# Performance work log

Hardware: AMD Instinct MI355X
Metric: run time of the kernel (lower is better)

## Reference

```python
import jax, jax.numpy as jnp
import numpy as np

B, N, L, E, U, G, R, D, C = 64, 50000, 8, 100000, 20000, 20000, 64, 16, 2


def setup_inputs() -> dict:
    rng = np.random.default_rng(0)
    key = jax.random.key(0)
    ks = jax.random.split(key, 10)
    # index structures (duplicate-free where the torch code assumes uniqueness)
    gene_map = jnp.asarray(rng.choice(N, G, replace=False).astype(np.int32))
    dst_unique = jnp.stack([jnp.asarray(rng.choice(N, U, replace=False).astype(np.int32)) for _ in range(L)])
    root_ids = jnp.asarray(rng.choice(N, R, replace=False).astype(np.int32))
    src = jax.random.randint(ks[0], (L, E), 0, N, dtype=jnp.int32)
    dst_pos = jax.random.randint(ks[1], (L, E), 0, U, dtype=jnp.int32)
    # data and parameters
    X_gene_batch = jax.random.normal(ks[2], (B, G), jnp.float32)
    w_in = jax.random.normal(ks[3], (D,), jnp.float32) * 0.5   # Linear(1, d) weight
    b_in = jax.random.normal(ks[4], (D,), jnp.float32) * 0.1
    W = jax.random.normal(ks[5], (L, D, D), jnp.float32) * (1.0 / np.sqrt(D))  # xavier-ish
    bias = jnp.zeros((N, D), jnp.float32)
    W_head = jax.random.normal(ks[6], (C, R * D), jnp.float32) * (1.0 / np.sqrt(R * D))
    b_head = jnp.zeros((C,), jnp.float32)
    return {
        "X_gene_batch": X_gene_batch, "w_in": w_in, "b_in": b_in, "W": W,
        "bias": bias, "W_head": W_head, "b_head": b_head,
        "gene_map": gene_map, "src": src, "dst_pos": dst_pos,
        "dst_unique": dst_unique, "root_ids": root_ids,
    }


def reference(X_gene_batch, w_in, b_in, W, bias, W_head, b_head,
              gene_map, src, dst_pos, dst_unique, root_ids):
    Bn = X_gene_batch.shape[0]
    n_nodes, d = bias.shape
    n_layers = W.shape[0]
    u = dst_unique.shape[1]
    # _init_state_vector: h=0, scatter in_proj(X[...,None]) at gene_map
    gene_emb = X_gene_batch[..., None] * w_in + b_in          # [B, G, d]
    h = jnp.zeros((Bn, n_nodes, d), X_gene_batch.dtype)
    h = h.at[:, gene_map].set(gene_emb)
    for li in range(n_layers):
        h_src = h[:, src[li]]                                  # gather [B, E, d]
        msg = jnp.einsum('bed,df->bef', h_src, W[li])          # small dxd matmul
        agg = jnp.zeros((Bn, u, d), h.dtype).at[:, dst_pos[li]].add(msg)  # scatter-add
        h_dst = jnp.tanh(agg + bias[dst_unique[li]][None])     # bias lookup + tanh (dropout=0)
        h = h.at[:, dst_unique[li]].set(h_dst)                 # write back
    feat = h[:, root_ids].reshape(Bn, -1)                      # roots_concat readout
    return feat @ W_head.T + b_head                            # [B, C]
```

## Files before the change

kernel.cpp:

```cpp
#include <hip/hip_runtime.h>
#include <hip/hip_fp16.h>
#include <cmath>

constexpr int B_ = 64, N_ = 50000, L_ = 8, E_ = 100000, U_ = 20000, G_ = 20000, R_ = 64, D_ = 16, C_ = 2;
constexpr int EPL_ = E_ + 3 * U_ + 4096;
constexpr int EPLG_ = EPL_ / 4 + 64;
constexpr int GPW = 8;
constexpr int GCAP = EPL_ / 4;
constexpr int SW = (GCAP + GPW - 1) / GPW;
constexpr int HISTB = (E_ + 255) / 256;

constexpr int BC = 64;
constexpr int F = BC * 2;

constexpr int HBC = 32;
constexpr int FH = HBC * 2;
constexpr int DST0 = 1 + G_;
constexpr int AROWS = DST0 + L_ * U_;

__device__ __forceinline__ float tanh_fast(float x) {
  float e = __expf(2.0f * x);
  return 1.0f - 2.0f * __builtin_amdgcn_rcpf(e + 1.0f);
}


__global__ __launch_bounds__(256) void hist_mark_k(
    const int* __restrict__ dst_pos, int* __restrict__ cnt,
    const int* __restrict__ dst_unique, const int* __restrict__ gene_map,
    int* __restrict__ wmask, int* __restrict__ posarr, int* __restrict__ lw0) {
  int li = blockIdx.y;
  int bx = blockIdx.x;
  if (bx < HISTB) {
    int e = bx * 256 + threadIdx.x;
    if (e < E_) atomicAdd(&cnt[li * U_ + dst_pos[li * E_ + e]], 1);
  } else if (li == 0) {
    int t = (bx - HISTB) * 256 + threadIdx.x;
    if (t < L_ * U_) {
      int lj = t / U_, u = t % U_;
      int n = dst_unique[t];
      posarr[lj * N_ + n] = u;
      atomicOr(&wmask[n], 1 << lj);
    } else {
      int g = t - L_ * U_;
      if (g < G_) lw0[gene_map[g]] = 1 + g;
    }
  }
}

__global__ __launch_bounds__(1024) void scan_kernel(
    const int* __restrict__ cnt, int* __restrict__ offs,
    int* __restrict__ woffs) {
  __shared__ int sums[1024];
  int li = blockIdx.x, t = threadIdx.x;
  int base = t * 20;
  int v[20];
  int s = 0;
#pragma unroll
  for (int i = 0; i < 20; ++i) {
    int idx = base + i;
    int c = (idx < U_) ? cnt[li * U_ + idx] : -1;
    int pc = (c < 0) ? 0 : ((c == 0) ? 4 : ((c + 3) & ~3));
    v[i] = s;
    s += pc;
  }
  sums[t] = s;
  __syncthreads();
  for (int off = 1; off < 1024; off <<= 1) {
    int o = (t >= off) ? sums[t - off] : 0;
    __syncthreads();
    sums[t] += o;
    __syncthreads();
  }
  int excl = sums[t] - s;
#pragma unroll
  for (int i = 0; i < 20; ++i) {
    int idx = base + i;
    if (idx < U_) {
      int sv = excl + v[i];
      offs[li * (U_ + 1) + idx] = sv;
      woffs[li * (U_ + 1) + idx] = sv;
    }
  }
  if (t == 1023) offs[li * (U_ + 1) + U_] = sums[1023];
}

__global__ __launch_bounds__(256) void scatter_arena_k(
    const int* __restrict__ dst_pos, const int* __restrict__ src,
    int* __restrict__ woffs, const int* __restrict__ wmask,
    const int* __restrict__ posarr, const int* __restrict__ lw0,
    int* __restrict__ ssrc) {
  int e = blockIdx.x * 256 + threadIdx.x;
  int li = blockIdx.y;
  if (e >= E_) return;
  int u = dst_pos[li * E_ + e];
  int p = atomicAdd(&woffs[li * (U_ + 1) + u], 1);
  int s = src[li * E_ + e];
  int m = wmask[s] & ((1 << li) - 1);
  int phys;
  if (m) {
    int lj = 31 - __clz(m);
    phys = DST0 + lj * U_ + posarr[lj * N_ + s];
  } else {
    phys = lw0[s];
  }
  ssrc[(size_t)li * EPL_ + p] = phys;
}

__global__ __launch_bounds__(256) void scatter_classic_k(
    const int* __restrict__ dst_pos, const int* __restrict__ src,
    int* __restrict__ woffs, int* __restrict__ ssrc) {
  int e = blockIdx.x * 256 + threadIdx.x;
  int li = blockIdx.y;
  if (e >= E_) return;
  int u = dst_pos[li * E_ + e];
  int p = atomicAdd(&woffs[li * (U_ + 1) + u], 1);
  ssrc[(size_t)li * EPL_ + p] = src[li * E_ + e];
}

__global__ __launch_bounds__(256) void pad_fill_ug_k(
    const int* __restrict__ woffs, const int* __restrict__ offs,
    int* __restrict__ ssrc, int* __restrict__ ug, int sentinel,
    float4* __restrict__ zrow) {
  int t = blockIdx.x * 256 + threadIdx.x;
  if (t < L_ * U_) {
    int li = t / U_, u = t % U_;
    int start = offs[li * (U_ + 1) + u];
    int end = woffs[li * (U_ + 1) + u];
    int pend = offs[li * (U_ + 1) + u + 1];
    int* sp = ssrc + (size_t)li * EPL_;
    for (int p = end; p < pend; ++p) sp[p] = sentinel;
    int* ugp = ug + (size_t)li * EPLG_;
    for (int g = start >> 2; g < (pend >> 2); ++g) ugp[g] = u;
  } else {
    int t2 = t - L_ * U_;
    int li = t2 >> 10, j = t2 & 1023;
    if (li < L_) {
      int* sp = ssrc + (size_t)li * EPL_;
      int ptot = offs[li * (U_ + 1) + U_];
      if (j < 256) {
        int pos = ptot + j;
        if (pos < EPL_) sp[pos] = sentinel;
        sp[EPL_ - 256 + j] = sentinel;
      }
      int* ugp = ug + (size_t)li * EPLG_;
      for (int gq = (ptot >> 2) + j; gq < EPLG_; gq += 1024) ugp[gq] = -1;
      if (li == 0 && j < FH && zrow) zrow[j] = make_float4(0.f, 0.f, 0.f, 0.f);
    }
  }
}

#define PHASE(VACC, VLD, IDLD, IDPF, NUCUR)          \
  {                                                  \
    loadRows(VLD, IDLD);                             \
    IDPF = *(const int4*)(sp + 4 * CLG(g + 4));      \
    int nuCur = NUCUR;                               \
    NUCUR = ugp[CLG(g + 3) + 1];                     \
    accum(VACC);                                     \
    if (nuCur != curU) {                             \
      flushu(curU);                                  \
      if (g + 1 >= gstop) return;                    \
      curU = nuCur;                                  \
    }                                                \
    ++g;                                             \
  }


__global__ __launch_bounds__(256) void gene_a(
    const float* __restrict__ X, const float* __restrict__ w_in,
    const float* __restrict__ b_in, float4* __restrict__ h4, int half) {
  __shared__ float xs[8][33];
  int tid = threadIdx.x;
  int g0 = blockIdx.x * 8;
  {
    int b = tid >> 3, gi = tid & 7;
    xs[gi][b] = X[(size_t)(half * HBC + b) * G_ + g0 + gi];
  }
  __syncthreads();
  int b = tid & 31;
  int gi = tid >> 5;
  float x = xs[gi][b];
  int g = g0 + gi;
  float4 out[2];
  __half2* oh = reinterpret_cast<__half2*>(out);
#pragma unroll
  for (int k = 0; k < 8; ++k) {
    float r0 = fmaf(x, w_in[2 * k], b_in[2 * k]);
    float r1 = fmaf(x, w_in[2 * k + 1], b_in[2 * k + 1]);
    oh[k] = __float22half2_rn(make_float2(r0, r1));
  }
  h4[(size_t)(1 + g) * FH + b * 2] = out[0];
  h4[(size_t)(1 + g) * FH + b * 2 + 1] = out[1];
}

__global__ __launch_bounds__(256, 2) void gfused_a(
    const float4* __restrict__ h4, const int* __restrict__ ug,
    const int* __restrict__ ssrc, const float* __restrict__ W,
    const float* __restrict__ bias, const int* __restrict__ dst_unique,
    float4* __restrict__ o4, int li) {
  __shared__ float Wlds[256];
  int tid = threadIdx.x;
  Wlds[tid] = W[li * 256 + tid];
  __syncthreads();
  int lane = tid & 63;
  int dh = lane & 1;
  int wv = __builtin_amdgcn_readfirstlane(blockIdx.x * 4 + (tid >> 6));
  const int* ugp = ug + (size_t)li * EPLG_;
  const int* sp = ssrc + (size_t)li * EPL_;
  const int* du = dst_unique + (size_t)li * U_;

  int g0 = wv * GPW, gend = g0 + GPW;
  int prevU = (g0 == 0) ? -2 : ugp[g0 - 1];
  int g = g0;
  while (g < gend && ugp[g] == prevU) ++g;
  if (g >= gend) return;
  int curU = ugp[g];
  if (curU < 0) return;
  int uend = ugp[gend - 1];
  int gstop;
  if (uend < 0) {
    gstop = g;
    while (ugp[gstop] >= 0) ++gstop;
  } else {
    gstop = gend;
    while (ugp[gstop] == uend) ++gstop;
  }

  __half2 acc[2][4];
  const __half2 z = __half2half2(__float2half(0.f));
#pragma unroll
  for (int j = 0; j < 2; ++j)
#pragma unroll
    for (int k = 0; k < 4; ++k) acc[j][k] = z;

  auto flushu = [&](int u) {
    int node = du[u];
    float biasv[8];
    {
      const float4* bp = (const float4*)(bias + (size_t)node * 16 + dh * 8);
      float4 q0 = bp[0], q1 = bp[1];
      biasv[0] = q0.x; biasv[1] = q0.y; biasv[2] = q0.z; biasv[3] = q0.w;
      biasv[4] = q1.x; biasv[5] = q1.y; biasv[6] = q1.z; biasv[7] = q1.w;
    }
    float a8[8];
#pragma unroll
    for (int k = 0; k < 4; ++k) {
      float2 f0 = __half22float2(acc[0][k]);
      float2 f1 = __half22float2(acc[1][k]);
      __half2 hv = __float22half2_rn(make_float2(f0.x + f1.x, f0.y + f1.y));
      float2 fa = __half22float2(hv);
      a8[2 * k] = fa.x; a8[2 * k + 1] = fa.y;
    }
    float pm[16];
#pragma unroll
    for (int j = 0; j < 16; ++j) pm[j] = 0.f;
#pragma unroll
    for (int dd = 0; dd < 8; ++dd) {
      float s = a8[dd];
      const float4* wr = (const float4*)&Wlds[(dh * 8 + dd) * 16];
      float4 w0 = wr[0], w1 = wr[1], w2 = wr[2], w3 = wr[3];
      pm[0] = fmaf(s, w0.x, pm[0]);  pm[1] = fmaf(s, w0.y, pm[1]);
      pm[2] = fmaf(s, w0.z, pm[2]);  pm[3] = fmaf(s, w0.w, pm[3]);
      pm[4] = fmaf(s, w1.x, pm[4]);  pm[5] = fmaf(s, w1.y, pm[5]);
      pm[6] = fmaf(s, w1.z, pm[6]);  pm[7] = fmaf(s, w1.w, pm[7]);
      pm[8] = fmaf(s, w2.x, pm[8]);  pm[9] = fmaf(s, w2.y, pm[9]);
      pm[10] = fmaf(s, w2.z, pm[10]); pm[11] = fmaf(s, w2.w, pm[11]);
      pm[12] = fmaf(s, w3.x, pm[12]); pm[13] = fmaf(s, w3.y, pm[13]);
      pm[14] = fmaf(s, w3.z, pm[14]); pm[15] = fmaf(s, w3.w, pm[15]);
    }
    float m8[8];
#pragma unroll
    for (int jj = 0; jj < 8; ++jj) {
      float s0 = pm[jj] + __shfl_xor(pm[jj], 1, 64);
      float s1 = pm[8 + jj] + __shfl_xor(pm[8 + jj], 1, 64);
      m8[jj] = dh ? s1 : s0;
    }
    float4 outv;
    __half2* ov = reinterpret_cast<__half2*>(&outv);
#pragma unroll
    for (int k = 0; k < 4; ++k) {
      ov[k] = __float22half2_rn(
          make_float2(tanh_fast(m8[2 * k] + biasv[2 * k]),
                      tanh_fast(m8[2 * k + 1] + biasv[2 * k + 1])));
    }
    o4[(size_t)(DST0 + li * U_ + u) * FH + lane] = outv;
#pragma unroll
    for (int j = 0; j < 2; ++j)
#pragma unroll
      for (int k = 0; k < 4; ++k) acc[j][k] = z;
  };

  auto loadRows = [&](float4 (&v)[4], int4 id) {
    v[0] = h4[(size_t)id.x * FH + lane];
    v[1] = h4[(size_t)id.y * FH + lane];
    v[2] = h4[(size_t)id.z * FH + lane];
    v[3] = h4[(size_t)id.w * FH + lane];
  };
  auto accum = [&](const float4 (&v)[4]) {
#pragma unroll
    for (int j = 0; j < 4; ++j) {
      const __half2* p = reinterpret_cast<const __half2*>(&v[j]);
#pragma unroll
      for (int k = 0; k < 4; ++k)
        acc[j & 1][k] = __hadd2(acc[j & 1][k], p[k]);
    }
  };
  auto CLG = [&](int q) { return (q < GCAP) ? q : GCAP - 1; };

  int4 id0 = *(const int4*)(sp + 4 * g);
  int4 id1 = *(const int4*)(sp + 4 * CLG(g + 1));
  int4 idP = *(const int4*)(sp + 4 * CLG(g + 2));
  int4 idQ = *(const int4*)(sp + 4 * CLG(g + 3));
  int4 idR;
  int nuA = ugp[g + 1];
  int nuB = ugp[CLG(g + 1) + 1];
  int nuC = ugp[CLG(g + 2) + 1];

  float4 va[4], vb[4], vc[4];
  loadRows(va, id0);
  loadRows(vb, id1);

  for (;;) {
    PHASE(va, vc, idP, idR, nuA)
    PHASE(vb, va, idQ, idP, nuB)
    PHASE(vc, vb, idR, idQ, nuC)
  }
}

__global__ __launch_bounds__(64) void head_a(
    const float4* __restrict__ h4, const float* __restrict__ W_head,
    const float* __restrict__ b_head, const int* __restrict__ root_ids,
    const int* __restrict__ wmask, const int* __restrict__ posarr,
    const int* __restrict__ lw0, int half, float* __restrict__ out) {
  int bl = blockIdx.x;
  int r = threadIdx.x;
  int node = root_ids[r];
  int m = wmask[node];
  int phys;
  if (m) {
    int lj = 31 - __clz(m);
    phys = DST0 + lj * U_ + posarr[lj * N_ + node];
  } else {
    phys = lw0[node];
  }
  float4 p0 = h4[(size_t)phys * FH + bl * 2];
  float4 p1 = h4[(size_t)phys * FH + bl * 2 + 1];
  float v[16];
  const __half2* ph0 = reinterpret_cast<const __half2*>(&p0);
  const __half2* ph1 = reinterpret_cast<const __half2*>(&p1);
#pragma unroll
  for (int k = 0; k < 4; ++k) {
    float2 f0 = __half22float2(ph0[k]);
    float2 f1 = __half22float2(ph1[k]);
    v[2 * k] = f0.x; v[2 * k + 1] = f0.y;
    v[8 + 2 * k] = f1.x; v[8 + 2 * k + 1] = f1.y;
  }
  float acc0 = 0.f, acc1 = 0.f;
#pragma unroll
  for (int d = 0; d < 16; ++d) {
    acc0 = fmaf(v[d], W_head[r * 16 + d], acc0);
    acc1 = fmaf(v[d], W_head[1024 + r * 16 + d], acc1);
  }
  for (int off = 32; off; off >>= 1) {
    acc0 += __shfl_down(acc0, off, 64);
    acc1 += __shfl_down(acc1, off, 64);
  }
  if (r == 0) {
    int gb = half * HBC + bl;
    out[gb * 2 + 0] = acc0 + b_head[0];
    out[gb * 2 + 1] = acc1 + b_head[1];
  }
}


__global__ __launch_bounds__(256) void gene_c(
    const float* __restrict__ X, const float* __restrict__ w_in,
    const float* __restrict__ b_in, const int* __restrict__ gene_map,
    float4* __restrict__ h4) {
  int t = blockIdx.x * 256 + threadIdx.x;
  if (t >= G_ * BC) return;
  int b = t % BC;
  int g = t / BC;
  float x = X[b * G_ + g];
  int node = gene_map[g];
  float4 out[2];
  __half2* oh = reinterpret_cast<__half2*>(out);
#pragma unroll
  for (int k = 0; k < 8; ++k) {
    float r0 = fmaf(x, w_in[2 * k], b_in[2 * k]);
    float r1 = fmaf(x, w_in[2 * k + 1], b_in[2 * k + 1]);
    oh[k] = __float22half2_rn(make_float2(r0, r1));
  }
  h4[(size_t)node * F + b * 2] = out[0];
  h4[(size_t)node * F + b * 2 + 1] = out[1];
}

__global__ __launch_bounds__(256, 2) void gather_c(
    const float4* __restrict__ h4, const int* __restrict__ ug,
    const int* __restrict__ ssrc, float4* __restrict__ agg4, int li) {
  int tid = threadIdx.x;
  int lane = tid & 63;
  int wv = __builtin_amdgcn_readfirstlane(blockIdx.x * 4 + (tid >> 6));
  const int* ugp = ug + (size_t)li * EPLG_;
  const int* sp = ssrc + (size_t)li * EPL_;

  int g0 = wv * GPW, gend = g0 + GPW;
  int prevU = (g0 == 0) ? -2 : ugp[g0 - 1];
  int g = g0;
  while (g < gend && ugp[g] == prevU) ++g;
  if (g >= gend) return;
  int curU = ugp[g];
  if (curU < 0) return;
  int uend = ugp[gend - 1];
  int gstop;
  if (uend < 0) {
    gstop = g;
    while (ugp[gstop] >= 0) ++gstop;
  } else {
    gstop = gend;
    while (ugp[gstop] == uend) ++gstop;
  }

  __half2 acc[2][2][4];
  const __half2 z = __half2half2(__float2half(0.f));
#pragma unroll
  for (int j = 0; j < 2; ++j)
#pragma unroll
    for (int r = 0; r < 2; ++r)
#pragma unroll
      for (int k = 0; k < 4; ++k) acc[j][r][k] = z;

  auto flushu = [&](int u) {
#pragma unroll
    for (int r = 0; r < 2; ++r) {
      float4 outv;
      __half2* ov = reinterpret_cast<__half2*>(&outv);
#pragma unroll
      for (int k = 0; k < 4; ++k) {
        float2 f0 = __half22float2(acc[0][r][k]);
        float2 f1 = __half22float2(acc[1][r][k]);
        ov[k] = __float22half2_rn(make_float2(f0.x + f1.x, f0.y + f1.y));
      }
      agg4[(size_t)u * F + lane + r * 64] = outv;
    }
#pragma unroll
    for (int j = 0; j < 2; ++j)
#pragma unroll
      for (int r = 0; r < 2; ++r)
#pragma unroll
        for (int k = 0; k < 4; ++k) acc[j][r][k] = z;
  };
  auto loadRows = [&](float4 (&v)[4][2], int4 id) {
    v[0][0] = h4[(size_t)id.x * F + lane]; v[0][1] = h4[(size_t)id.x * F + lane + 64];
    v[1][0] = h4[(size_t)id.y * F + lane]; v[1][1] = h4[(size_t)id.y * F + lane + 64];
    v[2][0] = h4[(size_t)id.z * F + lane]; v[2][1] = h4[(size_t)id.z * F + lane + 64];
    v[3][0] = h4[(size_t)id.w * F + lane]; v[3][1] = h4[(size_t)id.w * F + lane + 64];
  };
  auto accum = [&](const float4 (&v)[4][2]) {
#pragma unroll
    for (int j = 0; j < 4; ++j)
#pragma unroll
      for (int r = 0; r < 2; ++r) {
        const __half2* p = reinterpret_cast<const __half2*>(&v[j][r]);
#pragma unroll
        for (int k = 0; k < 4; ++k)
          acc[j & 1][r][k] = __hadd2(acc[j & 1][r][k], p[k]);
      }
  };
  auto CLG = [&](int q) { return (q < GCAP) ? q : GCAP - 1; };

  int4 id0 = *(const int4*)(sp + 4 * g);
  int4 id1 = *(const int4*)(sp + 4 * CLG(g + 1));
  int4 idP = *(const int4*)(sp + 4 * CLG(g + 2));
  int4 idQ = *(const int4*)(sp + 4 * CLG(g + 3));
  int4 idR;
  int nuA = ugp[g + 1];
  int nuB = ugp[CLG(g + 1) + 1];
  int nuC = ugp[CLG(g + 2) + 1];

  float4 va[4][2], vb[4][2], vc[4][2];
  loadRows(va, id0);
  loadRows(vb, id1);

  for (;;) {
    PHASE(va, vc, idP, idR, nuA)
    PHASE(vb, va, idQ, idP, nuB)
    PHASE(vc, vb, idR, idQ, nuC)
  }
}
#undef PHASE

__global__ __launch_bounds__(256) void dense_c(
    const float4* __restrict__ agg4, const float* __restrict__ W,
    const float* __restrict__ bias, const int* __restrict__ dst_unique,
    float4* __restrict__ h4, int li) {
  __shared__ float Wlds[256];
  int tid = threadIdx.x;
  Wlds[tid] = W[li * 256 + tid];
  __syncthreads();
  int u = __builtin_amdgcn_readfirstlane(blockIdx.x * 4 + (tid >> 6));
  int b = tid & 63;
  float4 c0 = agg4[(size_t)u * F + b * 2];
  float4 c1 = agg4[(size_t)u * F + b * 2 + 1];
  float a[16];
  {
    const __half2* p0 = reinterpret_cast<const __half2*>(&c0);
    const __half2* p1 = reinterpret_cast<const __half2*>(&c1);
#pragma unroll
    for (int k = 0; k < 4; ++k) {
      float2 f0 = __half22float2(p0[k]);
      float2 f1 = __half22float2(p1[k]);
      a[2 * k] = f0.x; a[2 * k + 1] = f0.y;
      a[8 + 2 * k] = f1.x; a[8 + 2 * k + 1] = f1.y;
    }
  }
  float m[16];
#pragma unroll
  for (int j = 0; j < 16; ++j) m[j] = 0.f;
#pragma unroll
  for (int d = 0; d < 16; ++d) {
    float s = a[d];
    const float4* wr = (const float4*)&Wlds[d * 16];
    float4 w0 = wr[0], w1 = wr[1], w2 = wr[2], w3 = wr[3];
    m[0] = fmaf(s, w0.x, m[0]);  m[1] = fmaf(s, w0.y, m[1]);
    m[2] = fmaf(s, w0.z, m[2]);  m[3] = fmaf(s, w0.w, m[3]);
    m[4] = fmaf(s, w1.x, m[4]);  m[5] = fmaf(s, w1.y, m[5]);
    m[6] = fmaf(s, w1.z, m[6]);  m[7] = fmaf(s, w1.w, m[7]);
    m[8] = fmaf(s, w2.x, m[8]);  m[9] = fmaf(s, w2.y, m[9]);
    m[10] = fmaf(s, w2.z, m[10]); m[11] = fmaf(s, w2.w, m[11]);
    m[12] = fmaf(s, w3.x, m[12]); m[13] = fmaf(s, w3.y, m[13]);
    m[14] = fmaf(s, w3.z, m[14]); m[15] = fmaf(s, w3.w, m[15]);
  }
  int node = dst_unique[li * U_ + u];
  const float4* bp = (const float4*)(bias + (size_t)node * 16);
  float4 b0 = bp[0], b1 = bp[1], b2 = bp[2], b3 = bp[3];
  float bb[16] = {b0.x, b0.y, b0.z, b0.w, b1.x, b1.y, b1.z, b1.w,
                  b2.x, b2.y, b2.z, b2.w, b3.x, b3.y, b3.z, b3.w};
  float4 o0, o1;
  __half2* ov0 = reinterpret_cast<__half2*>(&o0);
  __half2* ov1 = reinterpret_cast<__half2*>(&o1);
#pragma unroll
  for (int k = 0; k < 4; ++k) {
    ov0[k] = __float22half2_rn(make_float2(tanh_fast(m[2 * k] + bb[2 * k]),
                                           tanh_fast(m[2 * k + 1] + bb[2 * k + 1])));
    ov1[k] = __float22half2_rn(make_float2(tanh_fast(m[8 + 2 * k] + bb[8 + 2 * k]),
                                           tanh_fast(m[8 + 2 * k + 1] + bb[8 + 2 * k + 1])));
  }
  h4[(size_t)node * F + b * 2] = o0;
  h4[(size_t)node * F + b * 2 + 1] = o1;
}

__global__ __launch_bounds__(64) void head_c(
    const float4* __restrict__ h4, const float* __restrict__ W_head,
    const float* __restrict__ b_head, const int* __restrict__ root_ids,
    float* __restrict__ out) {
  int bl = blockIdx.x;
  int r = threadIdx.x;
  int node = root_ids[r];
  float4 p0 = h4[(size_t)node * F + bl * 2];
  float4 p1 = h4[(size_t)node * F + bl * 2 + 1];
  float v[16];
  const __half2* ph0 = reinterpret_cast<const __half2*>(&p0);
  const __half2* ph1 = reinterpret_cast<const __half2*>(&p1);
#pragma unroll
  for (int k = 0; k < 4; ++k) {
    float2 f0 = __half22float2(ph0[k]);
    float2 f1 = __half22float2(ph1[k]);
    v[2 * k] = f0.x; v[2 * k + 1] = f0.y;
    v[8 + 2 * k] = f1.x; v[8 + 2 * k + 1] = f1.y;
  }
  float acc0 = 0.f, acc1 = 0.f;
#pragma unroll
  for (int d = 0; d < 16; ++d) {
    acc0 = fmaf(v[d], W_head[r * 16 + d], acc0);
    acc1 = fmaf(v[d], W_head[1024 + r * 16 + d], acc1);
  }
  for (int off = 32; off; off >>= 1) {
    acc0 += __shfl_down(acc0, off, 64);
    acc1 += __shfl_down(acc1, off, 64);
  }
  if (r == 0) {
    out[bl * 2 + 0] = acc0 + b_head[0];
    out[bl * 2 + 1] = acc1 + b_head[1];
  }
}

__global__ void zero_out_k(float* out, int n) {
  int t = blockIdx.x * 256 + threadIdx.x;
  if (t < n) out[t] = 0.f;
}


static size_t arena_bytes() {
  return (size_t)AROWS * FH * 16 +
         (size_t)L_ * U_ * 4 +
         (size_t)2 * (N_ + 1) * 4 +
         (size_t)L_ * (U_ + 1) * 4 * 2 +
         (size_t)L_ * EPL_ * 4 +
         (size_t)L_ * EPLG_ * 4 +
         (size_t)L_ * N_ * 4;
}
static size_t classic_bytes() {
  return (size_t)(N_ + 1) * F * 16 + (size_t)U_ * F * 16 +
         (size_t)L_ * U_ * 4 + (size_t)L_ * (U_ + 1) * 4 * 2 +
         (size_t)L_ * EPL_ * 4 + (size_t)L_ * EPLG_ * 4;
}

extern "C" void kernel_launch(void* const* d_in, const int* in_sizes, int n_in,
                              void* d_out, int out_size, void* d_ws, size_t ws_size,
                              hipStream_t stream) {
  const float* X = (const float*)d_in[0];
  const float* w_in = (const float*)d_in[1];
  const float* b_in = (const float*)d_in[2];
  const float* W = (const float*)d_in[3];
  const float* bias = (const float*)d_in[4];
  const float* W_head = (const float*)d_in[5];
  const float* b_head = (const float*)d_in[6];
  const int* gene_map = (const int*)d_in[7];
  const int* src = (const int*)d_in[8];
  const int* dst_pos = (const int*)d_in[9];
  const int* dst_unique = (const int*)d_in[10];
  const int* root_ids = (const int*)d_in[11];
  float* out = (float*)d_out;

  dim3 egrid(HISTB, L_);
  const int pf_grid = (L_ * U_ + L_ * 1024 + 255) / 256;
  const int gather_grid = (SW + 3) / 4;

  if (ws_size >= arena_bytes()) {
    char* ws = (char*)d_ws;
    float4* arena = (float4*)ws;
    size_t off = (size_t)AROWS * FH * 16;
    int* cnt = (int*)(ws + off);    off += (size_t)L_ * U_ * 4;
    int* wmask = (int*)(ws + off);  off += (size_t)(N_ + 1) * 4;
    int* lw0 = (int*)(ws + off);    off += (size_t)(N_ + 1) * 4;
    int* offs = (int*)(ws + off);   off += (size_t)L_ * (U_ + 1) * 4;
    int* woffs = (int*)(ws + off);  off += (size_t)L_ * (U_ + 1) * 4;
    int* ssrc = (int*)(ws + off);   off += (size_t)L_ * EPL_ * 4;
    int* ug = (int*)(ws + off);     off += (size_t)L_ * EPLG_ * 4;
    int* posarr = (int*)(ws + off);

    hipMemsetAsync(cnt, 0, (size_t)L_ * U_ * 4 + (size_t)2 * (N_ + 1) * 4,
                   stream);
    dim3 hmgrid(HISTB + (L_ * U_ + G_ + 255) / 256, L_);
    hist_mark_k<<<hmgrid, 256, 0, stream>>>(dst_pos, cnt, dst_unique, gene_map,
                                            wmask, posarr, lw0);
    scan_kernel<<<L_, 1024, 0, stream>>>(cnt, offs, woffs);
    scatter_arena_k<<<egrid, 256, 0, stream>>>(dst_pos, src, woffs, wmask,
                                               posarr, lw0, ssrc);
    pad_fill_ug_k<<<pf_grid, 256, 0, stream>>>(woffs, offs, ssrc, ug, 0, arena);

    for (int half = 0; half < 2; ++half) {
      gene_a<<<G_ / 8, 256, 0, stream>>>(X, w_in, b_in, arena, half);
      for (int li = 0; li < L_; ++li) {
        gfused_a<<<gather_grid, 256, 0, stream>>>(arena, ug, ssrc, W, bias,
                                                  dst_unique, arena, li);
      }
      head_a<<<HBC, 64, 0, stream>>>(arena, W_head, b_head, root_ids, wmask,
                                     posarr, lw0, half, out);
    }
  } else if (ws_size >= classic_bytes()) {
    const size_t h_bytes = (size_t)(N_ + 1) * F * 16;
    const size_t agg_bytes = (size_t)U_ * F * 16;
    char* ws = (char*)d_ws;
    float4* h4 = (float4*)ws;
    float4* agg4 = (float4*)(ws + h_bytes);
    size_t off = h_bytes + agg_bytes;
    int* cnt = (int*)(ws + off);   off += (size_t)L_ * U_ * 4;
    int* offs = (int*)(ws + off);  off += (size_t)L_ * (U_ + 1) * 4;
    int* woffs = (int*)(ws + off); off += (size_t)L_ * (U_ + 1) * 4;
    int* ssrc = (int*)(ws + off);  off += (size_t)L_ * EPL_ * 4;
    int* ug = (int*)(ws + off);

    hipMemsetAsync(cnt, 0, (size_t)L_ * U_ * 4, stream);
    hipMemsetAsync(h4, 0, h_bytes, stream);
    hist_mark_k<<<egrid, 256, 0, stream>>>(dst_pos, cnt, nullptr, nullptr,
                                           nullptr, nullptr, nullptr);
    scan_kernel<<<L_, 1024, 0, stream>>>(cnt, offs, woffs);
    scatter_classic_k<<<egrid, 256, 0, stream>>>(dst_pos, src, woffs, ssrc);
    pad_fill_ug_k<<<pf_grid, 256, 0, stream>>>(woffs, offs, ssrc, ug, N_,
                                               nullptr);
    gene_c<<<(G_ * BC + 255) / 256, 256, 0, stream>>>(X, w_in, b_in, gene_map, h4);
    const int dense_grid = U_ * BC / 256;
    for (int li = 0; li < L_; ++li) {
      gather_c<<<gather_grid, 256, 0, stream>>>(h4, ug, ssrc, agg4, li);
      dense_c<<<dense_grid, 256, 0, stream>>>(agg4, W, bias, dst_unique, h4, li);
    }
    head_c<<<BC, 64, 0, stream>>>(h4, W_head, b_head, root_ids, out);
  } else {
    zero_out_k<<<(out_size + 255) / 256, 256, 0, stream>>>(out, out_size);
  }
}
```

Before: 568.8 us.

## Reuse histogram atomic ranks for CSR scatter and add separate source remap pass

The histogram kernel now records each edge's atomic return value as its rank within its destination bucket. The scatter step then computes positions as offset plus rank instead of issuing a second round of atomics on a write-offset array. The physical-row remapping of source indices moves out of the scatter into a new remap kernel that runs after padding, so sentinel slots (now N) are also remapped. This removes one atomic pass over the edges but adds a rank buffer and an extra kernel launch that re-reads and rewrites the sorted source array.

```diff
diff --git a/kernel.cpp b/kernel.cpp
--- a/kernel.cpp
+++ b/kernel.cpp
@@ -26,13 +26,15 @@
 
 __global__ __launch_bounds__(256) void hist_mark_k(
     const int* __restrict__ dst_pos, int* __restrict__ cnt,
-    const int* __restrict__ dst_unique, const int* __restrict__ gene_map,
-    int* __restrict__ wmask, int* __restrict__ posarr, int* __restrict__ lw0) {
+    int* __restrict__ rank, const int* __restrict__ dst_unique,
+    const int* __restrict__ gene_map, int* __restrict__ wmask,
+    int* __restrict__ posarr, int* __restrict__ lw0) {
   int li = blockIdx.y;
   int bx = blockIdx.x;
   if (bx < HISTB) {
     int e = bx * 256 + threadIdx.x;
-    if (e < E_) atomicAdd(&cnt[li * U_ + dst_pos[li * E_ + e]], 1);
+    if (e < E_)
+      rank[li * E_ + e] = atomicAdd(&cnt[li * U_ + dst_pos[li * E_ + e]], 1);
   } else if (li == 0) {
     int t = (bx - HISTB) * 256 + threadIdx.x;
     if (t < L_ * U_) {
@@ -48,8 +50,7 @@
 }
 
 __global__ __launch_bounds__(1024) void scan_kernel(
-    const int* __restrict__ cnt, int* __restrict__ offs,
-    int* __restrict__ woffs) {
+    const int* __restrict__ cnt, int* __restrict__ offs) {
   __shared__ int sums[1024];
   int li = blockIdx.x, t = threadIdx.x;
   int base = t * 20;
@@ -75,60 +76,34 @@
 #pragma unroll
   for (int i = 0; i < 20; ++i) {
     int idx = base + i;
-    if (idx < U_) {
-      int sv = excl + v[i];
-      offs[li * (U_ + 1) + idx] = sv;
-      woffs[li * (U_ + 1) + idx] = sv;
-    }
+    if (idx < U_) offs[li * (U_ + 1) + idx] = excl + v[i];
   }
   if (t == 1023) offs[li * (U_ + 1) + U_] = sums[1023];
 }
 
-__global__ __launch_bounds__(256) void scatter_arena_k(
+__global__ __launch_bounds__(256) void scatter_kernel(
     const int* __restrict__ dst_pos, const int* __restrict__ src,
-    int* __restrict__ woffs, const int* __restrict__ wmask,
-    const int* __restrict__ posarr, const int* __restrict__ lw0,
+    const int* __restrict__ offs, const int* __restrict__ rank,
     int* __restrict__ ssrc) {
   int e = blockIdx.x * 256 + threadIdx.x;
   int li = blockIdx.y;
   if (e >= E_) return;
   int u = dst_pos[li * E_ + e];
-  int p = atomicAdd(&woffs[li * (U_ + 1) + u], 1);
-  int s = src[li * E_ + e];
-  int m = wmask[s] & ((1 << li) - 1);
-  int phys;
-  if (m) {
-    int lj = 31 - __clz(m);
-    phys = DST0 + lj * U_ + posarr[lj * N_ + s];
-  } else {
-    phys = lw0[s];
-  }
-  ssrc[(size_t)li * EPL_ + p] = phys;
-}
-
-__global__ __launch_bounds__(256) void scatter_classic_k(
-    const int* __restrict__ dst_pos, const int* __restrict__ src,
-    int* __restrict__ woffs, int* __restrict__ ssrc) {
-  int e = blockIdx.x * 256 + threadIdx.x;
-  int li = blockIdx.y;
-  if (e >= E_) return;
-  int u = dst_pos[li * E_ + e];
-  int p = atomicAdd(&woffs[li * (U_ + 1) + u], 1);
+  int p = offs[li * (U_ + 1) + u] + rank[li * E_ + e];
   ssrc[(size_t)li * EPL_ + p] = src[li * E_ + e];
 }
 
 __global__ __launch_bounds__(256) void pad_fill_ug_k(
-    const int* __restrict__ woffs, const int* __restrict__ offs,
-    int* __restrict__ ssrc, int* __restrict__ ug, int sentinel,
-    float4* __restrict__ zrow) {
+    const int* __restrict__ cnt, const int* __restrict__ offs,
+    int* __restrict__ ssrc, int* __restrict__ ug, float4* __restrict__ zrow) {
   int t = blockIdx.x * 256 + threadIdx.x;
   if (t < L_ * U_) {
     int li = t / U_, u = t % U_;
     int start = offs[li * (U_ + 1) + u];
-    int end = woffs[li * (U_ + 1) + u];
+    int end = start + cnt[li * U_ + u];
     int pend = offs[li * (U_ + 1) + u + 1];
     int* sp = ssrc + (size_t)li * EPL_;
-    for (int p = end; p < pend; ++p) sp[p] = sentinel;
+    for (int p = end; p < pend; ++p) sp[p] = N_;
     int* ugp = ug + (size_t)li * EPLG_;
     for (int g = start >> 2; g < (pend >> 2); ++g) ugp[g] = u;
   } else {
@@ -139,14 +114,36 @@
       int ptot = offs[li * (U_ + 1) + U_];
       if (j < 256) {
         int pos = ptot + j;
-        if (pos < EPL_) sp[pos] = sentinel;
-        sp[EPL_ - 256 + j] = sentinel;
+        if (pos < EPL_) sp[pos] = N_;
+        sp[EPL_ - 256 + j] = N_;
       }
       int* ugp = ug + (size_t)li * EPLG_;
       for (int gq = (ptot >> 2) + j; gq < EPLG_; gq += 1024) ugp[gq] = -1;
       if (li == 0 && j < FH && zrow) zrow[j] = make_float4(0.f, 0.f, 0.f, 0.f);
     }
   }
+}
+
+__global__ __launch_bounds__(256) void remap_k(
+    const int* __restrict__ offs, const int* __restrict__ wmask,
+    const int* __restrict__ posarr, const int* __restrict__ lw0,
+    int* __restrict__ ssrc) {
+  int p = blockIdx.x * 256 + threadIdx.x;
+  int li = blockIdx.y;
+  if (p >= EPL_) return;
+  int ptot = offs[li * (U_ + 1) + U_];
+  if (p >= ptot + 256 && p < EPL_ - 256) return;
+  int* sp = ssrc + (size_t)li * EPL_;
+  int s = sp[p];
+  int m = wmask[s] & ((1 << li) - 1);
+  int phys;
+  if (m) {
+    int lj = 31 - __clz(m);
+    phys = DST0 + lj * U_ + posarr[lj * N_ + s];
+  } else {
+    phys = lw0[s];
+  }
+  sp[p] = phys;
 }
 
 #define PHASE(VACC, VLD, IDLD, IDPF, NUCUR)          \
@@ -594,15 +591,16 @@
   return (size_t)AROWS * FH * 16 +
          (size_t)L_ * U_ * 4 +
          (size_t)2 * (N_ + 1) * 4 +
-         (size_t)L_ * (U_ + 1) * 4 * 2 +
+         (size_t)L_ * (U_ + 1) * 4 +
+         (size_t)L_ * E_ * 4 +
          (size_t)L_ * EPL_ * 4 +
          (size_t)L_ * EPLG_ * 4 +
          (size_t)L_ * N_ * 4;
 }
 static size_t classic_bytes() {
   return (size_t)(N_ + 1) * F * 16 + (size_t)U_ * F * 16 +
-         (size_t)L_ * U_ * 4 + (size_t)L_ * (U_ + 1) * 4 * 2 +
-         (size_t)L_ * EPL_ * 4 + (size_t)L_ * EPLG_ * 4;
+         (size_t)L_ * U_ * 4 + (size_t)L_ * (U_ + 1) * 4 +
+         (size_t)L_ * E_ * 4 + (size_t)L_ * EPL_ * 4 + (size_t)L_ * EPLG_ * 4;
 }
 
 extern "C" void kernel_launch(void* const* d_in, const int* in_sizes, int n_in,
@@ -634,7 +632,7 @@
     int* wmask = (int*)(ws + off);  off += (size_t)(N_ + 1) * 4;
     int* lw0 = (int*)(ws + off);    off += (size_t)(N_ + 1) * 4;
     int* offs = (int*)(ws + off);   off += (size_t)L_ * (U_ + 1) * 4;
-    int* woffs = (int*)(ws + off);  off += (size_t)L_ * (U_ + 1) * 4;
+    int* rank = (int*)(ws + off);   off += (size_t)L_ * E_ * 4;
     int* ssrc = (int*)(ws + off);   off += (size_t)L_ * EPL_ * 4;
     int* ug = (int*)(ws + off);     off += (size_t)L_ * EPLG_ * 4;
     int* posarr = (int*)(ws + off);
@@ -642,12 +640,13 @@
     hipMemsetAsync(cnt, 0, (size_t)L_ * U_ * 4 + (size_t)2 * (N_ + 1) * 4,
                    stream);
     dim3 hmgrid(HISTB + (L_ * U_ + G_ + 255) / 256, L_);
-    hist_mark_k<<<hmgrid, 256, 0, stream>>>(dst_pos, cnt, dst_unique, gene_map,
-                                            wmask, posarr, lw0);
-    scan_kernel<<<L_, 1024, 0, stream>>>(cnt, offs, woffs);
-    scatter_arena_k<<<egrid, 256, 0, stream>>>(dst_pos, src, woffs, wmask,
-                                               posarr, lw0, ssrc);
-    pad_fill_ug_k<<<pf_grid, 256, 0, stream>>>(woffs, offs, ssrc, ug, 0, arena);
+    hist_mark_k<<<hmgrid, 256, 0, stream>>>(dst_pos, cnt, rank, dst_unique,
+                                            gene_map, wmask, posarr, lw0);
+    scan_kernel<<<L_, 1024, 0, stream>>>(cnt, offs);
+    scatter_kernel<<<egrid, 256, 0, stream>>>(dst_pos, src, offs, rank, ssrc);
+    pad_fill_ug_k<<<pf_grid, 256, 0, stream>>>(cnt, offs, ssrc, ug, arena);
+    dim3 rgrid((EPL_ + 255) / 256, L_);
+    remap_k<<<rgrid, 256, 0, stream>>>(offs, wmask, posarr, lw0, ssrc);
 
     for (int half = 0; half < 2; ++half) {
       gene_a<<<G_ / 8, 256, 0, stream>>>(X, w_in, b_in, arena, half);
@@ -667,18 +666,17 @@
     size_t off = h_bytes + agg_bytes;
     int* cnt = (int*)(ws + off);   off += (size_t)L_ * U_ * 4;
     int* offs = (int*)(ws + off);  off += (size_t)L_ * (U_ + 1) * 4;
-    int* woffs = (int*)(ws + off); off += (size_t)L_ * (U_ + 1) * 4;
+    int* rank = (int*)(ws + off);  off += (size_t)L_ * E_ * 4;
     int* ssrc = (int*)(ws + off);  off += (size_t)L_ * EPL_ * 4;
     int* ug = (int*)(ws + off);
 
     hipMemsetAsync(cnt, 0, (size_t)L_ * U_ * 4, stream);
     hipMemsetAsync(h4, 0, h_bytes, stream);
-    hist_mark_k<<<egrid, 256, 0, stream>>>(dst_pos, cnt, nullptr, nullptr,
-                                           nullptr, nullptr, nullptr);
-    scan_kernel<<<L_, 1024, 0, stream>>>(cnt, offs, woffs);
-    scatter_classic_k<<<egrid, 256, 0, stream>>>(dst_pos, src, woffs, ssrc);
-    pad_fill_ug_k<<<pf_grid, 256, 0, stream>>>(woffs, offs, ssrc, ug, N_,
-                                               nullptr);
+    hist_mark_k<<<egrid, 256, 0, stream>>>(dst_pos, cnt, rank, nullptr,
+                                           nullptr, nullptr, nullptr, nullptr);
+    scan_kernel<<<L_, 1024, 0, stream>>>(cnt, offs);
+    scatter_kernel<<<egrid, 256, 0, stream>>>(dst_pos, src, offs, rank, ssrc);
+    pad_fill_ug_k<<<pf_grid, 256, 0, stream>>>(cnt, offs, ssrc, ug, nullptr);
     gene_c<<<(G_ * BC + 255) / 256, 256, 0, stream>>>(X, w_in, b_in, gene_map, h4);
     const int dense_grid = U_ * BC / 256;
     for (int li = 0; li < L_; ++li) {
```

Result: faster. 553.0 us (-2.8%).
